# Optimization experiments

Measured on AMD Instinct MI355X. Metric: run time of the kernel, lower is better.

The kernel has to match this reference:

```python
import jax, jax.numpy as jnp
import numpy as np

T, B = 21, 4096
H, E, V = 1024, 50, 96
PAD = 0


def setup_inputs() -> dict:
    key = jax.random.key(0)
    ks = jax.random.split(key, 10)
    s_e = 1.0 / np.sqrt(H)  # torch LSTM init scale
    emb = jax.random.normal(ks[0], (V, E), jnp.float32)
    emb = emb.at[PAD].set(0.0)  # padding_idx row is zero
    return {
        "input_ids": jax.random.randint(ks[1], (T, B), 0, V),
        "h0": jax.random.normal(ks[2], (1, B, H), jnp.float32),
        "c0": jax.random.normal(ks[3], (1, B, H), jnp.float32),
        "emb": emb,
        "W_ih": jax.random.uniform(ks[4], (4 * H, E), jnp.float32, -s_e, s_e),
        "W_hh": jax.random.uniform(ks[5], (4 * H, H), jnp.float32, -s_e, s_e),
        "b_ih": jax.random.uniform(ks[6], (4 * H,), jnp.float32, -s_e, s_e),
        "b_hh": jax.random.uniform(ks[7], (4 * H,), jnp.float32, -s_e, s_e),
        "W_out": jax.random.uniform(ks[8], (V, H), jnp.float32, -s_e, s_e),
        "b_out": jax.random.uniform(ks[9], (V,), jnp.float32, -s_e, s_e),
    }


def reference(input_ids, h0, c0, emb, W_ih, W_hh, b_ih, b_hh, W_out, b_out):
    # char_embeds: (T, B, E)
    x = emb[input_ids]
    # Precompute input projections for all timesteps in one GEMM: (T, B, 4H)
    x_proj = jnp.einsum("tbe,ge->tbg", x, W_ih) + b_ih + b_hh

    def step(carry, xp_t):
        h, c = carry  # (B, H) each
        gates = xp_t + h @ W_hh.T  # (B, 4H), torch gate order i,f,g,o
        i, f, g, o = jnp.split(gates, 4, axis=-1)
        i = jax.nn.sigmoid(i)
        f = jax.nn.sigmoid(f)
        g = jnp.tanh(g)
        o = jax.nn.sigmoid(o)
        c = f * c + i * g
        h = o * jnp.tanh(c)
        return (h, c), h

    (h_T, c_T), h_ts = jax.lax.scan(step, (h0[0], c0[0]), x_proj)
    # char_output_projection: (T, B, V)
    scores = jnp.einsum("tbh,vh->tbv", h_ts, W_out) + b_out
    return scores, (h_T[None], c_T[None])
```

## Files before the change

kernel.cpp:

```cpp
#include <hip/hip_runtime.h>
#include <hip/hip_bf16.h>


#define T_STEPS 21
#define BSZ 4096
#define HDIM 1024
#define VOCAB 96
#define EDIM 50

typedef __attribute__((ext_vector_type(8))) short short8;
typedef __attribute__((ext_vector_type(4))) float f32x4;

#define GLL16(g, l)                                                        \
  __builtin_amdgcn_global_load_lds(                                        \
      (const __attribute__((address_space(1))) void*)(g),                  \
      (__attribute__((address_space(3))) void*)(l), 16, 0, 0)

#define ASM_BARRIER() asm volatile("s_barrier" ::: "memory")
#define ASM_VMCNT4() asm volatile("s_waitcnt vmcnt(4)" ::: "memory")
#define ASM_VMCNT0() asm volatile("s_waitcnt vmcnt(0)" ::: "memory")

__device__ __forceinline__ float sigmoidf_fast(float x) {
  return 1.0f / (1.0f + __expf(-x));
}
__device__ __forceinline__ float tanhf_fast(float x) {
  return 2.0f / (1.0f + __expf(-2.0f * x)) - 1.0f;
}

__global__ void prep_convert(const float* __restrict__ Whh_f,
                             const float* __restrict__ Wout_f,
                             const float* __restrict__ h0,
                             __hip_bfloat16* __restrict__ Whh,
                             __hip_bfloat16* __restrict__ Wout,
                             __hip_bfloat16* __restrict__ hb0) {
  int idx = blockIdx.x * 256 + threadIdx.x;
  if (idx < 4 * HDIM * HDIM) {
    Whh[idx] = __float2bfloat16(Whh_f[idx]);
    hb0[idx] = __float2bfloat16(h0[idx]);
  }
  if (idx < VOCAB * HDIM) Wout[idx] = __float2bfloat16(Wout_f[idx]);
}

__global__ void prep_ptable(const float* __restrict__ emb,
                            const float* __restrict__ Wih,
                            const float* __restrict__ bih,
                            const float* __restrict__ bhh,
                            __hip_bfloat16* __restrict__ Pb) {
  int idx = blockIdx.x * 256 + threadIdx.x;
  int v = idx >> 12, g = idx & 4095;
  int gate = g >> 10, j = g & 1023;
  const float* er = emb + v * EDIM;
  const float* wr = Wih + g * EDIM;
  float s = bih[g] + bhh[g];
#pragma unroll 10
  for (int e = 0; e < EDIM; ++e) s += er[e] * wr[e];
  Pb[(size_t)(j >> 6) * 24576 + v * 256 + gate * 64 + (j & 63)] =
      __float2bfloat16(s);
}


#define STAGE_A(h, kt, b)                                                   \
  do {                                                                      \
    GLL16(hprev + aSrc[0] + (size_t)(h) * 131072 + (size_t)(kt) * 64,       \
          smem + ((b) << 16) + ((h) << 14) + aDst[0]);                      \
    GLL16(hprev + aSrc[1] + (size_t)(h) * 131072 + (size_t)(kt) * 64,       \
          smem + ((b) << 16) + ((h) << 14) + aDst[1]);                      \
  } while (0)

#define STAGE_B(h, kt, b)                                                   \
  do {                                                                      \
    GLL16(Whh + bSrc[h][0] + (size_t)(kt) * 64,                             \
          smem + ((b) << 16) + bDst[h][0]);                                 \
    GLL16(Whh + bSrc[h][1] + (size_t)(kt) * 64,                             \
          smem + ((b) << 16) + bDst[h][1]);                                 \
  } while (0)

#define PHASE(mh, nh, STAGE_STMT, VM_STMT)                                  \
  {                                                                         \
    const int sl0 = ((k16q) ^ u7) * 8;                                      \
    const int sl1 = ((4 + k16q) ^ u7) * 8;                                  \
    short8 af0[4], bf0[2];                                                  \
    _Pragma("unroll") for (int mi2 = 0; mi2 < 4; ++mi2)                     \
        af0[mi2] = *(const short8*)&cA[((mh) * 128 + wr * 64 + mi2 * 16 +   \
                                        u16) * 64 + sl0];                   \
    _Pragma("unroll") for (int ni2 = 0; ni2 < 2; ++ni2)                     \
        bf0[ni2] = *(const short8*)&cB[(wc * 64 + (nh) * 32 + ni2 * 16 +    \
                                        u16) * 64 + sl0];                   \
    STAGE_STMT;                                                             \
    ASM_BARRIER();                                                          \
    __builtin_amdgcn_s_setprio(1);                                          \
    short8 af1[4], bf1[2];                                                  \
    _Pragma("unroll") for (int mi2 = 0; mi2 < 4; ++mi2)                     \
        af1[mi2] = *(const short8*)&cA[((mh) * 128 + wr * 64 + mi2 * 16 +   \
                                        u16) * 64 + sl1];                   \
    _Pragma("unroll") for (int ni2 = 0; ni2 < 2; ++ni2)                     \
        bf1[ni2] = *(const short8*)&cB[(wc * 64 + (nh) * 32 + ni2 * 16 +    \
                                        u16) * 64 + sl1];                   \
    _Pragma("unroll") for (int mi2 = 0; mi2 < 4; ++mi2)                     \
        _Pragma("unroll") for (int ni2 = 0; ni2 < 2; ++ni2)                 \
            acc[(mh) * 4 + mi2][(nh) * 2 + ni2] =                           \
                __builtin_amdgcn_mfma_f32_16x16x32_bf16(                    \
                    af0[mi2], bf0[ni2],                                     \
                    acc[(mh) * 4 + mi2][(nh) * 2 + ni2], 0, 0, 0);          \
    _Pragma("unroll") for (int mi2 = 0; mi2 < 4; ++mi2)                     \
        _Pragma("unroll") for (int ni2 = 0; ni2 < 2; ++ni2)                 \
            acc[(mh) * 4 + mi2][(nh) * 2 + ni2] =                           \
                __builtin_amdgcn_mfma_f32_16x16x32_bf16(                    \
                    af1[mi2], bf1[ni2],                                     \
                    acc[(mh) * 4 + mi2][(nh) * 2 + ni2], 0, 0, 0);          \
    __builtin_amdgcn_s_setprio(0);                                          \
    VM_STMT;                                                                \
    __builtin_amdgcn_sched_barrier(0);                                      \
    ASM_BARRIER();                                                          \
  }

template <bool LAST>
__global__ __launch_bounds__(512, 2) void lstm_step_kernel(
    const int* __restrict__ ids,
    const __hip_bfloat16* __restrict__ hprev,
    const __hip_bfloat16* __restrict__ Whh,
    const __hip_bfloat16* __restrict__ Pb,
    const float* __restrict__ c_in,
    float* __restrict__ c_out,
    __hip_bfloat16* __restrict__ hnext,
    float* __restrict__ hf32)
{
  __shared__ __align__(16) char smem[131072];

  const int tid = threadIdx.x;
  const int wid = tid >> 6;
  const int lane = tid & 63;
  const int wr = wid >> 2;
  const int wc = wid & 3;
  const int u16 = lane & 15;
  const int k16q = lane >> 4;
  const int u7 = u16 & 7;

  const int bid = blockIdx.x;
  const int mt = (bid & 7) * 2 + ((bid >> 3) & 1);
  const int jt = bid >> 4;
  const int m0 = mt * 256;

  const int lrow = lane >> 3;
  const int swcol = ((lane & 7) ^ lrow) * 8;

  size_t aSrc[2];
  size_t bSrc[2][2];
  int aDst[2];
  int bDst[2][2];
#pragma unroll
  for (int q = 0; q < 2; ++q) {
    const int g = wid * 2 + q;
    aSrc[q] = (size_t)(m0 + g * 8 + lrow) * HDIM + swcol;
    aDst[q] = g * 1024;
#pragma unroll
    for (int h = 0; h < 2; ++h) {
      const int R = (g >> 2) * 64 + h * 32 + (g & 3) * 8;
      const int n = R + lrow;
      const int gate = (n >> 4) & 3;
      const int uo = (n >> 6) * 16 + (n & 15);
      bSrc[h][q] = (size_t)(gate * HDIM + jt * 64 + uo) * HDIM + swcol;
      bDst[h][q] = 32768 + R * 128;
    }
  }

  STAGE_A(0, 0, 0);
  STAGE_B(0, 0, 0);
  STAGE_A(1, 0, 0);
  STAGE_B(1, 0, 0);

  const int jcol = jt * 64 + wc * 16 + u16;
  float cpre[8][4];
#pragma unroll
  for (int mi = 0; mi < 8; ++mi)
#pragma unroll
    for (int r = 0; r < 4; ++r)
      cpre[mi][r] = c_in[(size_t)(m0 + (mi >> 2) * 128 + wr * 64 +
                                  (mi & 3) * 16 + k16q * 4 + r) *
                             HDIM +
                         jcol];

  STAGE_A(0, 1, 1);
  STAGE_B(0, 1, 1);

  ASM_VMCNT4();
  ASM_BARRIER();

  f32x4 acc[8][4] = {};

#pragma unroll 2
  for (int k = 0; k < 16; ++k) {
    const int b = k & 1;
    const int nb = b ^ 1;
    const __hip_bfloat16* cA = (const __hip_bfloat16*)(smem + (b << 16));
    const __hip_bfloat16* cB =
        (const __hip_bfloat16*)(smem + (b << 16) + 32768);
    PHASE(0, 0, { if (k < 15) STAGE_A(1, k + 1, nb); }, {});
    PHASE(0, 1, { if (k < 15) STAGE_B(1, k + 1, nb); }, {});
    PHASE(1, 0, { if (k < 14) STAGE_A(0, k + 2, b); }, {});
    PHASE(1, 1, { if (k < 14) STAGE_B(0, k + 2, b); }, {
      if (k < 14) {
        ASM_VMCNT4();
      } else if (k == 14) {
        ASM_VMCNT0();
      }
    });
  }

  {
    const __hip_bfloat16* Pbj = Pb + (size_t)jt * 24576;
#pragma unroll
    for (int i = 0; i < 6; ++i)
      GLL16(Pbj + (wid * 6 + i) * 512 + lane * 8,
            smem + (wid * 6 + i) * 1024);
  }
  ASM_VMCNT0();
  ASM_BARRIER();

  const __hip_bfloat16* sPb = (const __hip_bfloat16*)smem;
  const int rb = m0 + wr * 64 + k16q * 4;
#pragma unroll
  for (int mi = 0; mi < 8; ++mi) {
#pragma unroll
    for (int r = 0; r < 4; ++r) {
      const int row = rb + (mi >> 2) * 128 + (mi & 3) * 16 + r;
      const int id = ids[row];
      const __hip_bfloat16* Pr = &sPb[id * 256 + wc * 16 + u16];
      float iv = acc[mi][0][r] + __bfloat162float(Pr[0]);
      float fv = acc[mi][1][r] + __bfloat162float(Pr[64]);
      float gv = acc[mi][2][r] + __bfloat162float(Pr[128]);
      float ov = acc[mi][3][r] + __bfloat162float(Pr[192]);
      iv = sigmoidf_fast(iv);
      fv = sigmoidf_fast(fv);
      gv = tanhf_fast(gv);
      ov = sigmoidf_fast(ov);
      const size_t off = (size_t)row * HDIM + jcol;
      const float cc = fv * cpre[mi][r] + iv * gv;
      c_out[off] = cc;
      const float hh = ov * tanhf_fast(cc);
      hnext[off] = __float2bfloat16(hh);
      if (LAST) hf32[off] = hh;
    }
  }
}

__global__ __launch_bounds__(256, 2) void scores_kernel(
    const __hip_bfloat16* __restrict__ h,
    const __hip_bfloat16* __restrict__ Wout,
    const float* __restrict__ bout,
    float* __restrict__ out)
{
  __shared__ __align__(16) __hip_bfloat16 sA[128 * 128];
  __shared__ __align__(16) __hip_bfloat16 sB[96 * 128];

  const int tid = threadIdx.x;
  const int wave = tid >> 6, lane = tid & 63;
  const int u16 = lane & 15, k16q = lane >> 4;
  const long r0 = (long)blockIdx.x * 128;

  f32x4 acc[2][6] = {};

  const int srow4 = lane >> 4;
  const int sslot = lane & 15;

  for (int k0 = 0; k0 < HDIM; k0 += 128) {
#pragma unroll
    for (int i = 0; i < 8; ++i) {
      int row = wave * 32 + i * 4 + srow4;
      int gg = sslot ^ (row & 15);
      GLL16(h + (r0 + row) * HDIM + k0 + gg * 8,
            &sA[(wave * 32 + i * 4) * 128]);
    }
#pragma unroll
    for (int i = 0; i < 6; ++i) {
      int row = wave * 24 + i * 4 + srow4;
      int gg = sslot ^ (row & 15);
      GLL16(Wout + (size_t)row * HDIM + k0 + gg * 8,
            &sB[(wave * 24 + i * 4) * 128]);
    }
    __syncthreads();
#pragma unroll
    for (int kk = 0; kk < 128; kk += 32) {
      const int sl = (((kk >> 3) + k16q) ^ u16) * 8;
      short8 af[2], bf[6];
#pragma unroll
      for (int mi = 0; mi < 2; ++mi)
        af[mi] = *(const short8*)&sA[(wave * 32 + mi * 16 + u16) * 128 + sl];
#pragma unroll
      for (int ni = 0; ni < 6; ++ni)
        bf[ni] = *(const short8*)&sB[(ni * 16 + u16) * 128 + sl];
#pragma unroll
      for (int mi = 0; mi < 2; ++mi)
#pragma unroll
        for (int ni = 0; ni < 6; ++ni)
          acc[mi][ni] = __builtin_amdgcn_mfma_f32_16x16x32_bf16(
              af[mi], bf[ni], acc[mi][ni], 0, 0, 0);
    }
    __syncthreads();
  }

#pragma unroll
  for (int ni = 0; ni < 6; ++ni) {
    int v = ni * 16 + u16;
    float bv = bout[v];
#pragma unroll
    for (int mi = 0; mi < 2; ++mi)
#pragma unroll
      for (int r = 0; r < 4; ++r) {
        long grow = r0 + wave * 32 + mi * 16 + k16q * 4 + r;
        out[grow * VOCAB + v] = acc[mi][ni][r] + bv;
      }
  }
}

extern "C" void kernel_launch(void* const* d_in, const int* in_sizes, int n_in,
                              void* d_out, int out_size, void* d_ws,
                              size_t ws_size, hipStream_t stream) {
  const int* ids = (const int*)d_in[0];
  const float* h0 = (const float*)d_in[1];
  const float* c0 = (const float*)d_in[2];
  const float* emb = (const float*)d_in[3];
  const float* Wih = (const float*)d_in[4];
  const float* Whh_f = (const float*)d_in[5];
  const float* bih = (const float*)d_in[6];
  const float* bhh = (const float*)d_in[7];
  const float* Wout_f = (const float*)d_in[8];
  const float* bout = (const float*)d_in[9];

  float* out = (float*)d_out;
  float* scores = out;
  float* hT = out + (size_t)T_STEPS * BSZ * VOCAB;
  float* cT = hT + (size_t)BSZ * HDIM;

  const size_t BH = (size_t)BSZ * HDIM;
  char* w = (char*)d_ws;
  __hip_bfloat16* Pb = (__hip_bfloat16*)w;   w += (size_t)16 * 24576 * 2;
  __hip_bfloat16* Whh = (__hip_bfloat16*)w;  w += (size_t)4 * HDIM * HDIM * 2;
  __hip_bfloat16* Wout = (__hip_bfloat16*)w; w += (size_t)VOCAB * HDIM * 2;
  __hip_bfloat16* hts = (__hip_bfloat16*)w;
  size_t base = (size_t)16 * 24576 * 2 + (size_t)4 * HDIM * HDIM * 2 +
                (size_t)VOCAB * HDIM * 2;
  const bool full = ws_size >= base + (size_t)(T_STEPS + 1) * BH * 2;

  prep_convert<<<dim3((4 * HDIM * HDIM + 255) / 256), dim3(256), 0, stream>>>(
      Whh_f, Wout_f, h0, Whh, Wout, hts);
  prep_ptable<<<dim3((VOCAB * 4096) / 256), dim3(256), 0, stream>>>(
      emb, Wih, bih, bhh, Pb);

  for (int t = 0; t < T_STEPS; ++t) {
    __hip_bfloat16* hp = hts + (full ? (size_t)t * BH : (size_t)(t & 1) * BH);
    __hip_bfloat16* hn =
        hts + (full ? (size_t)(t + 1) * BH : (size_t)((t + 1) & 1) * BH);
    const float* cin = (t == 0) ? c0 : cT;
    if (t == T_STEPS - 1) {
      lstm_step_kernel<true><<<dim3(256), dim3(512), 0, stream>>>(
          ids + (size_t)t * BSZ, hp, Whh, Pb, cin, cT, hn, hT);
    } else {
      lstm_step_kernel<false><<<dim3(256), dim3(512), 0, stream>>>(
          ids + (size_t)t * BSZ, hp, Whh, Pb, cin, cT, hn, nullptr);
    }
    if (!full) {
      scores_kernel<<<dim3(BSZ / 128), dim3(256), 0, stream>>>(
          hn, Wout, bout, scores + (size_t)t * BSZ * VOCAB);
    }
  }
  if (full) {
    scores_kernel<<<dim3(T_STEPS * BSZ / 128), dim3(256), 0, stream>>>(
        hts + BH, Wout, bout, scores);
  }
}
```

Before: 1.336 ms.

## Reuse A/B register fragments across MFMA quadrants and interleave P-table gates

The inner k-loop is restructured so each quadrant's A and B fragments are loaded from LDS once and reused across two MFMA quadrants in a snake order (00, 01, 11, 10). Previously each of the four phases reloaded both A and B fragments. This cuts LDS read traffic per k-step at the cost of more live vector registers. Separately, the precomputed input-projection table now stores the four gates for a hidden unit contiguously, so the epilogue fetches them with one 8-byte LDS load instead of four scalar loads.

New measurement: 1.435 ms. 7.4% more time.

```diff
diff --git a/kernel.cpp b/kernel.cpp
--- a/kernel.cpp
+++ b/kernel.cpp
@@ -9,6 +9,7 @@
 #define EDIM 50
 
 typedef __attribute__((ext_vector_type(8))) short short8;
+typedef __attribute__((ext_vector_type(4))) short shortx4;
 typedef __attribute__((ext_vector_type(4))) float f32x4;
 
 #define GLL16(g, l)                                                        \
@@ -25,6 +26,9 @@
 }
 __device__ __forceinline__ float tanhf_fast(float x) {
   return 2.0f / (1.0f + __expf(-2.0f * x)) - 1.0f;
+}
+__device__ __forceinline__ float b2f(short s) {
+  return __uint_as_float(((unsigned int)(unsigned short)s) << 16);
 }
 
 __global__ void prep_convert(const float* __restrict__ Whh_f,
@@ -54,7 +58,7 @@
   float s = bih[g] + bhh[g];
 #pragma unroll 10
   for (int e = 0; e < EDIM; ++e) s += er[e] * wr[e];
-  Pb[(size_t)(j >> 6) * 24576 + v * 256 + gate * 64 + (j & 63)] =
+  Pb[(size_t)(j >> 6) * 24576 + v * 256 + (j & 63) * 4 + gate] =
       __float2bfloat16(s);
 }
 
@@ -75,44 +79,38 @@
           smem + ((b) << 16) + bDst[h][1]);                                 \
   } while (0)
 
-#define PHASE(mh, nh, STAGE_STMT, VM_STMT)                                  \
-  {                                                                         \
-    const int sl0 = ((k16q) ^ u7) * 8;                                      \
-    const int sl1 = ((4 + k16q) ^ u7) * 8;                                  \
-    short8 af0[4], bf0[2];                                                  \
+#define LOAD_A(dst, mh)                                                     \
+  _Pragma("unroll") for (int mi2 = 0; mi2 < 4; ++mi2) {                     \
+    dst[mi2] = *(const short8*)&cA[((mh) * 128 + wr * 64 + mi2 * 16 +       \
+                                    u16) * 64 + sl0];                       \
+    dst[4 + mi2] = *(const short8*)&cA[((mh) * 128 + wr * 64 + mi2 * 16 +   \
+                                        u16) * 64 + sl1];                   \
+  }
+
+#define LOAD_B(dst, nh)                                                     \
+  _Pragma("unroll") for (int ni2 = 0; ni2 < 2; ++ni2) {                     \
+    dst[ni2] = *(const short8*)&cB[(wc * 64 + (nh) * 32 + ni2 * 16 +        \
+                                    u16) * 64 + sl0];                       \
+    dst[2 + ni2] = *(const short8*)&cB[(wc * 64 + (nh) * 32 + ni2 * 16 +    \
+                                        u16) * 64 + sl1];                   \
+  }
+
+#define MFMA_Q(mh, nh, A, Bv)                                               \
+  do {                                                                      \
+    __builtin_amdgcn_s_setprio(1);                                          \
     _Pragma("unroll") for (int mi2 = 0; mi2 < 4; ++mi2)                     \
-        af0[mi2] = *(const short8*)&cA[((mh) * 128 + wr * 64 + mi2 * 16 +   \
-                                        u16) * 64 + sl0];                   \
-    _Pragma("unroll") for (int ni2 = 0; ni2 < 2; ++ni2)                     \
-        bf0[ni2] = *(const short8*)&cB[(wc * 64 + (nh) * 32 + ni2 * 16 +    \
-                                        u16) * 64 + sl0];                   \
-    STAGE_STMT;                                                             \
-    ASM_BARRIER();                                                          \
-    __builtin_amdgcn_s_setprio(1);                                          \
-    short8 af1[4], bf1[2];                                                  \
-    _Pragma("unroll") for (int mi2 = 0; mi2 < 4; ++mi2)                     \
-        af1[mi2] = *(const short8*)&cA[((mh) * 128 + wr * 64 + mi2 * 16 +   \
-                                        u16) * 64 + sl1];                   \
-    _Pragma("unroll") for (int ni2 = 0; ni2 < 2; ++ni2)                     \
-        bf1[ni2] = *(const short8*)&cB[(wc * 64 + (nh) * 32 + ni2 * 16 +    \
-                                        u16) * 64 + sl1];                   \
-    _Pragma("unroll") for (int mi2 = 0; mi2 < 4; ++mi2)                     \
-        _Pragma("unroll") for (int ni2 = 0; ni2 < 2; ++ni2)                 \
-            acc[(mh) * 4 + mi2][(nh) * 2 + ni2] =                           \
-                __builtin_amdgcn_mfma_f32_16x16x32_bf16(                    \
-                    af0[mi2], bf0[ni2],                                     \
-                    acc[(mh) * 4 + mi2][(nh) * 2 + ni2], 0, 0, 0);          \
-    _Pragma("unroll") for (int mi2 = 0; mi2 < 4; ++mi2)                     \
-        _Pragma("unroll") for (int ni2 = 0; ni2 < 2; ++ni2)                 \
-            acc[(mh) * 4 + mi2][(nh) * 2 + ni2] =                           \
-                __builtin_amdgcn_mfma_f32_16x16x32_bf16(                    \
-                    af1[mi2], bf1[ni2],                                     \
-                    acc[(mh) * 4 + mi2][(nh) * 2 + ni2], 0, 0, 0);          \
+        _Pragma("unroll") for (int ni2 = 0; ni2 < 2; ++ni2) {               \
+      acc[(mh) * 4 + mi2][(nh) * 2 + ni2] =                                 \
+          __builtin_amdgcn_mfma_f32_16x16x32_bf16(                          \
+              A[mi2], Bv[ni2], acc[(mh) * 4 + mi2][(nh) * 2 + ni2],         \
+              0, 0, 0);                                                     \
+      acc[(mh) * 4 + mi2][(nh) * 2 + ni2] =                                 \
+          __builtin_amdgcn_mfma_f32_16x16x32_bf16(                          \
+              A[4 + mi2], Bv[2 + ni2],                                      \
+              acc[(mh) * 4 + mi2][(nh) * 2 + ni2], 0, 0, 0);                \
+    }                                                                       \
     __builtin_amdgcn_s_setprio(0);                                          \
-    VM_STMT;                                                                \
-    __builtin_amdgcn_sched_barrier(0);                                      \
-    ASM_BARRIER();                                                          \
-  }
+  } while (0)
 
 template <bool LAST>
 __global__ __launch_bounds__(512, 2) void lstm_step_kernel(
@@ -135,6 +133,8 @@
   const int u16 = lane & 15;
   const int k16q = lane >> 4;
   const int u7 = u16 & 7;
+  const int sl0 = (k16q ^ u7) * 8;
+  const int sl1 = ((4 + k16q) ^ u7) * 8;
 
   const int bid = blockIdx.x;
   const int mt = (bid & 7) * 2 + ((bid >> 3) & 1);
@@ -195,16 +195,36 @@
     const __hip_bfloat16* cA = (const __hip_bfloat16*)(smem + (b << 16));
     const __hip_bfloat16* cB =
         (const __hip_bfloat16*)(smem + (b << 16) + 32768);
-    PHASE(0, 0, { if (k < 15) STAGE_A(1, k + 1, nb); }, {});
-    PHASE(0, 1, { if (k < 15) STAGE_B(1, k + 1, nb); }, {});
-    PHASE(1, 0, { if (k < 14) STAGE_A(0, k + 2, b); }, {});
-    PHASE(1, 1, { if (k < 14) STAGE_B(0, k + 2, b); }, {
-      if (k < 14) {
-        ASM_VMCNT4();
-      } else if (k == 14) {
-        ASM_VMCNT0();
-      }
-    });
+    short8 a0[8], a1[8], b0[4], b1[4];
+
+    LOAD_A(a0, 0);
+    LOAD_B(b0, 0);
+    if (k < 15) STAGE_A(1, k + 1, nb);
+    ASM_BARRIER();
+    MFMA_Q(0, 0, a0, b0);
+    ASM_BARRIER();
+
+    LOAD_B(b1, 1);
+    if (k < 15) STAGE_B(1, k + 1, nb);
+    ASM_BARRIER();
+    MFMA_Q(0, 1, a0, b1);
+    ASM_BARRIER();
+
+    LOAD_A(a1, 1);
+    if (k < 14) STAGE_A(0, k + 2, b);
+    ASM_BARRIER();
+    MFMA_Q(1, 1, a1, b1);
+    ASM_BARRIER();
+
+    if (k < 14) STAGE_B(0, k + 2, b);
+    ASM_BARRIER();
+    MFMA_Q(1, 0, a1, b0);
+    if (k < 14) {
+      ASM_VMCNT4();
+    } else if (k == 14) {
+      ASM_VMCNT0();
+    }
+    ASM_BARRIER();
   }
 
   {
@@ -218,6 +238,7 @@
   ASM_BARRIER();
 
   const __hip_bfloat16* sPb = (const __hip_bfloat16*)smem;
+  const int uo4 = (wc * 16 + u16) * 4;
   const int rb = m0 + wr * 64 + k16q * 4;
 #pragma unroll
   for (int mi = 0; mi < 8; ++mi) {
@@ -225,11 +246,11 @@
     for (int r = 0; r < 4; ++r) {
       const int row = rb + (mi >> 2) * 128 + (mi & 3) * 16 + r;
       const int id = ids[row];
-      const __hip_bfloat16* Pr = &sPb[id * 256 + wc * 16 + u16];
-      float iv = acc[mi][0][r] + __bfloat162float(Pr[0]);
-      float fv = acc[mi][1][r] + __bfloat162float(Pr[64]);
-      float gv = acc[mi][2][r] + __bfloat162float(Pr[128]);
-      float ov = acc[mi][3][r] + __bfloat162float(Pr[192]);
+      const shortx4 pv = *(const shortx4*)&sPb[id * 256 + uo4];
+      float iv = acc[mi][0][r] + b2f(pv[0]);
+      float fv = acc[mi][1][r] + b2f(pv[1]);
+      float gv = acc[mi][2][r] + b2f(pv[2]);
+      float ov = acc[mi][3][r] + b2f(pv[3]);
       iv = sigmoidf_fast(iv);
       fv = sigmoidf_fast(fv);
       gv = tanhf_fast(gv);
```
